# Kernel tuning notes

Hardware: AMD Instinct MI355X
Metric: run time of the kernel (lower is better)

The kernel has to match this reference:

```python
import jax, jax.numpy as jnp
import numpy as np

SINKHORN_ITERS = 20
SINKHORN_TEMP = 0.2


def log_sinkhorn(log_alpha, n_iters=SINKHORN_ITERS, temperature=SINKHORN_TEMP):
    """Log-domain Sinkhorn normalization over the last two dims."""
    log_alpha = log_alpha / temperature
    for _ in range(n_iters):
        log_alpha = log_alpha - jax.nn.logsumexp(log_alpha, axis=-1, keepdims=True)
        log_alpha = log_alpha - jax.nn.logsumexp(log_alpha, axis=-2, keepdims=True)
    return jnp.exp(log_alpha)


def setup_inputs() -> dict:
    key = jax.random.key(0)
    k_x, k_a, k_w1, k_wv = jax.random.split(key, 4)
    B = 64
    N, K, BASIS = 1024, 64, 8
    # xavier-uniform-like init scales
    a_bound = np.sqrt(6.0 / (N + N))
    w1_bound = np.sqrt(6.0 / (N + BASIS))
    wv_bound = np.sqrt(6.0 / (K + K))
    x = jax.random.normal(k_x, (B, N * K), dtype=jnp.float32)
    A_logits = jax.random.uniform(k_a, (N, N), dtype=jnp.float32, minval=-a_bound, maxval=a_bound)
    W_1 = jax.random.uniform(k_w1, (N, BASIS), dtype=jnp.float32, minval=-w1_bound, maxval=w1_bound)
    W_V = jax.random.uniform(k_wv, (BASIS, K, K), dtype=jnp.float32, minval=-wv_bound, maxval=wv_bound)
    return {"x": x, "A_logits": A_logits, "W_1": W_1, "W_V": W_V}


def reference(x, A_logits, W_1, W_V):
    B = x.shape[0]
    N, K = A_logits.shape[0], W_V.shape[-1]
    # Doubly-stochastic global mixing matrix A: [N, N]
    A = log_sinkhorn(A_logits)
    # Local block logits via basis combination: [N, K, K]
    W_logits = jnp.einsum('tk,kde->tde', W_1, W_V)
    W = log_sinkhorn(W_logits)
    x_reshaped = x.reshape(B, N, K)
    x_local = jnp.einsum('bni,nio->bno', x_reshaped, W)   # per-block KxK mix
    x_global = jnp.einsum('mn,bno->bmo', A, x_local)       # NxN block mix
    return x_global.reshape(B, N * K)
```

## Files before the change

kernel.cpp:

```cpp
#include <hip/hip_runtime.h>
#include <hip/hip_bf16.h>


#define N_DIM 1024
#define INV_T 5.0f
#define ABLK 32

typedef __attribute__((ext_vector_type(8))) short short8;
typedef __attribute__((ext_vector_type(4))) float float4v;

__device__ __forceinline__ float wave_red_sum(float x) {
#define DPP_ADD(C)                                                            \
  {                                                                           \
    int _y = __builtin_amdgcn_update_dpp(0, __float_as_int(x), (C), 0xf, 0xf, \
                                         true);                               \
    x += __int_as_float(_y);                                                  \
  }
  DPP_ADD(0x111);
  DPP_ADD(0x112);
  DPP_ADD(0x114);
  DPP_ADD(0x118);
  DPP_ADD(0x142);
  DPP_ADD(0x143);
#undef DPP_ADD
  return x;
}

__global__ __launch_bounds__(256, 2) void k_front(
    const float* __restrict__ x, const float* __restrict__ L,
    const float* __restrict__ W1, const float* __restrict__ WV,
    float* __restrict__ E0, __hip_bfloat16* __restrict__ Eh,
    __hip_bfloat16* __restrict__ El, float* __restrict__ P,
    unsigned* __restrict__ ctrl, float* __restrict__ u_g,
    float* __restrict__ v_g, float* __restrict__ XL, int write_bf16) {
  __shared__ __align__(16) float smem[5136];
  const int t = threadIdx.x;
  const int bid = blockIdx.x;
  const int lane = t & 63;
  const int w = t >> 6;
  (void)ctrl;

  if (bid < ABLK) {
    float* v_s = smem;
    float* red = smem + 1024;
    const int b = bid;
    const int r0 = b * 32;

    float e[8][16];
#pragma unroll
    for (int j = 0; j < 8; ++j) {
      const int r = r0 + 8 * w + j;
      const float* Lr = L + (size_t)r * N_DIM + lane;
#pragma unroll
      for (int k = 0; k < 16; ++k) e[j][k] = __expf(Lr[k * 64] * INV_T);
      if (write_bf16) {
        __hip_bfloat16* EhR = Eh + (size_t)r * N_DIM + lane;
        __hip_bfloat16* ElR = El + (size_t)r * N_DIM + lane;
#pragma unroll
        for (int k = 0; k < 16; ++k) {
          __hip_bfloat16 h = __float2bfloat16(e[j][k]);
          EhR[k * 64] = h;
          ElR[k * 64] = __float2bfloat16(e[j][k] - __bfloat162float(h));
        }
      } else {
        float* ER = E0 + (size_t)r * N_DIM + lane;
#pragma unroll
        for (int k = 0; k < 16; ++k) ER[k * 64] = e[j][k];
      }
    }
    v_s[t] = 1.0f;
    v_s[t + 256] = 1.0f;
    v_s[t + 512] = 1.0f;
    v_s[t + 768] = 1.0f;
    __syncthreads();

    for (int it = 0; it < 20; ++it) {
      float vv[16];
#pragma unroll
      for (int k = 0; k < 16; ++k) vv[k] = v_s[k * 64 + lane];
      float u[8];
#pragma unroll
      for (int j = 0; j < 8; ++j) {
        float p = 0.f;
#pragma unroll
        for (int k = 0; k < 16; ++k) p += e[j][k] * vv[k];
        p = wave_red_sum(p);
        u[j] = 1.0f /
               __int_as_float(__builtin_amdgcn_readlane(__float_as_int(p), 63));
      }
#pragma unroll
      for (int k = 0; k < 16; ++k) {
        float cpl = e[0][k] * u[0] + e[1][k] * u[1] + e[2][k] * u[2] +
                    e[3][k] * u[3] + e[4][k] * u[4] + e[5][k] * u[5] +
                    e[6][k] * u[6] + e[7][k] * u[7];
        red[w * 1028 + k * 64 + lane] = cpl;
      }
      if (it == 19 && lane == 0) {
#pragma unroll
        for (int j = 0; j < 8; ++j) u_g[r0 + 8 * w + j] = u[j];
      }
      __syncthreads();
      float* Pit = P + (size_t)it * (ABLK * N_DIM);
      float cp4[4];
#pragma unroll
      for (int cc = 0; cc < 4; ++cc) {
        const int c = t + cc * 256;
        cp4[cc] = red[c] + red[1028 + c] + red[2 * 1028 + c] + red[3 * 1028 + c];
        __hip_atomic_store(&Pit[b * N_DIM + c], cp4[cc], __ATOMIC_RELAXED,
                           __HIP_MEMORY_SCOPE_AGENT);
      }
      for (int cc = 0; cc < 4; ++cc) {
        const int c = t + cc * 256;
        unsigned vals[ABLK];
#pragma unroll
        for (int pb = 0; pb < ABLK; ++pb)
          vals[pb] =
              __hip_atomic_load((const unsigned*)&Pit[pb * N_DIM + c],
                                __ATOMIC_RELAXED, __HIP_MEMORY_SCOPE_AGENT);
        for (;;) {
          unsigned miss = 0u;
#pragma unroll
          for (int pb = 0; pb < ABLK; ++pb) miss |= (vals[pb] == 0u) ? 1u : 0u;
          if (miss == 0u) break;
#pragma unroll
          for (int pb = 0; pb < ABLK; ++pb)
            if (vals[pb] == 0u)
              vals[pb] = __hip_atomic_load(
                  (const unsigned*)&Pit[pb * N_DIM + c], __ATOMIC_RELAXED,
                  __HIP_MEMORY_SCOPE_AGENT);
        }
        float s2 = 0.f;
#pragma unroll
        for (int pb = 0; pb < ABLK; ++pb) s2 += __uint_as_float(vals[pb]);
        v_s[c] = 1.0f / s2;
      }
      __syncthreads();
    }
    if (b == 0) {
#pragma unroll
      for (int cc = 0; cc < 4; ++cc) v_g[t + cc * 256] = v_s[t + cc * 256];
    }
    return;
  }

  float* ug = smem + w * 64;
  const int n = (bid - ABLK) * 4 + w;

  const int pidx = lane << 2;

  float w1[8];
#pragma unroll
  for (int k = 0; k < 8; ++k) w1[k] = W1[n * 8 + k];
  float e[64];
#pragma unroll
  for (int i = 0; i < 64; ++i) {
    float acc = 0.f;
#pragma unroll
    for (int k = 0; k < 8; ++k) acc += w1[k] * WV[k * 4096 + i * 64 + lane];
    e[i] = __expf(acc * INV_T);
  }

  float v = 1.0f;
  for (int it = 0; it < 20; ++it) {
    float a[32];
    {
      const bool hi = (lane & 32) != 0;
      const int pj = pidx ^ (32 << 2);
#pragma unroll
      for (int j = 0; j < 32; ++j) {
        float s0 = (hi ? e[j] : e[j + 32]) * v;
        float k0 = (hi ? e[j + 32] : e[j]) * v;
        a[j] = k0 + __int_as_float(__builtin_amdgcn_ds_bpermute(
                        pj, __float_as_int(s0)));
      }
    }
#define BSTAGE(D)                                                          \
  {                                                                        \
    const bool hi = (lane & (D)) != 0;                                     \
    const int pj = pidx ^ ((D) << 2);                                      \
    _Pragma("unroll") for (int j = 0; j < (D); ++j) {                      \
      float s0 = hi ? a[j] : a[j + (D)];                                   \
      float k0 = hi ? a[j + (D)] : a[j];                                   \
      a[j] = k0 + __int_as_float(                                          \
                      __builtin_amdgcn_ds_bpermute(pj, __float_as_int(s0))); \
    }                                                                      \
  }
    BSTAGE(16)
    BSTAGE(8)
    BSTAGE(4)
    BSTAGE(2)
    BSTAGE(1)
#undef BSTAGE
    const float u_l = 1.0f / a[0];
    ug[lane] = u_l;
    float s2 = 0.f;
#pragma unroll
    for (int q = 0; q < 16; ++q) {
      float4 u4 = *(const float4*)&ug[4 * q];
      s2 += e[4 * q] * u4.x + e[4 * q + 1] * u4.y + e[4 * q + 2] * u4.z +
            e[4 * q + 3] * u4.w;
    }
    v = 1.0f / s2;
  }

#pragma unroll
  for (int q = 0; q < 16; ++q) {
    float4 u4 = *(const float4*)&ug[4 * q];
    e[4 * q] *= u4.x;
    e[4 * q + 1] *= u4.y;
    e[4 * q + 2] *= u4.z;
    e[4 * q + 3] *= u4.w;
  }

  const float* xn = x + (size_t)n * 64;
  float* xl = XL + (size_t)n * 4096;
#pragma unroll 4
  for (int bb = 0; bb < 64; ++bb) {
    const float* xr = xn + (size_t)bb * 65536;
    float acc = 0.f;
#pragma unroll
    for (int q = 0; q < 16; ++q) {
      float4 xb = *(const float4*)&xr[4 * q];
      acc += xb.x * e[4 * q] + xb.y * e[4 * q + 1] + xb.z * e[4 * q + 2] +
             xb.w * e[4 * q + 3];
    }
    xl[bb * 64 + lane] = acc * v;
  }
}

__global__ __launch_bounds__(256) void k_xt(const float* __restrict__ XL,
                                            const float* __restrict__ v_g,
                                            __hip_bfloat16* __restrict__ XTh,
                                            __hip_bfloat16* __restrict__ XTl) {
  __shared__ float T[64 * 68];
  __shared__ float vsh[64];
  const int t = threadIdx.x;
  const int n0 = blockIdx.x * 64;
  const int c0 = blockIdx.y * 64;
  if (t < 64) vsh[t] = v_g[n0 + t];
  {
    const int r = t >> 4;
    const int c4 = (t & 15) * 4;
#pragma unroll
    for (int p = 0; p < 4; ++p) {
      float4 f =
          *(const float4*)&XL[(size_t)(n0 + r + 16 * p) * 4096 + c0 + c4];
      *(float4*)&T[(r + 16 * p) * 68 + c4] = f;
    }
  }
  __syncthreads();
  const int cl = t >> 2;
  const int nb = (t & 3) * 16;
  __align__(16) __hip_bfloat16 hbuf[16];
  __align__(16) __hip_bfloat16 lbuf[16];
#pragma unroll
  for (int j = 0; j < 16; ++j) {
    float xv = T[(nb + j) * 68 + cl] * vsh[nb + j];
    __hip_bfloat16 h = __float2bfloat16(xv);
    hbuf[j] = h;
    lbuf[j] = __float2bfloat16(xv - __bfloat162float(h));
  }
  const size_t off = (size_t)(c0 + cl) * 1024 + n0 + nb;
  *(uint4*)&XTh[off] = *(uint4*)&hbuf[0];
  *(uint4*)&XTh[off + 8] = *(uint4*)&hbuf[8];
  *(uint4*)&XTl[off] = *(uint4*)&lbuf[0];
  *(uint4*)&XTl[off + 8] = *(uint4*)&lbuf[8];
}

#define LSTR 72
__global__ __launch_bounds__(256) void k_gemm3(
    const ushort* __restrict__ Eh, const ushort* __restrict__ El,
    const ushort* __restrict__ XTh, const ushort* __restrict__ XTl,
    const float* __restrict__ u_g, float* __restrict__ out) {
  __shared__ ushort As[128 * LSTR];
  __shared__ ushort Xs[128 * LSTR];
  __shared__ float ush[128];
  const int t = threadIdx.x;
  const int m0 = blockIdx.x * 128;
  const int c0 = blockIdx.y * 128;
  const int wid = t >> 6, lane = t & 63;
  const int wm = (wid & 1) * 64, wc = (wid >> 1) * 64;
  const int lm = lane & 15, q = lane >> 4;
  const int sr = t >> 1;
  const int sc = (t & 1) * 32;
  if (t < 128) ush[t] = u_g[m0 + t];

  float4v acc[4][4];
#pragma unroll
  for (int i = 0; i < 4; ++i)
#pragma unroll
    for (int j = 0; j < 4; ++j) acc[i][j] = (float4v){0.f, 0.f, 0.f, 0.f};

  for (int seg = 0; seg < 3; ++seg) {
    const ushort* Ag = (seg == 1) ? El : Eh;
    const ushort* Xg = (seg == 2) ? XTl : XTh;
    for (int k0 = 0; k0 < 1024; k0 += 64) {
      __syncthreads();
      const ushort* ag = Ag + (size_t)(m0 + sr) * 1024 + k0 + sc;
      const ushort* xg = Xg + (size_t)(c0 + sr) * 1024 + k0 + sc;
      uint4 a0 = *(const uint4*)(ag);
      uint4 a1 = *(const uint4*)(ag + 8);
      uint4 a2 = *(const uint4*)(ag + 16);
      uint4 a3 = *(const uint4*)(ag + 24);
      uint4 x0 = *(const uint4*)(xg);
      uint4 x1 = *(const uint4*)(xg + 8);
      uint4 x2 = *(const uint4*)(xg + 16);
      uint4 x3 = *(const uint4*)(xg + 24);
      *(uint4*)&As[sr * LSTR + sc] = a0;
      *(uint4*)&As[sr * LSTR + sc + 8] = a1;
      *(uint4*)&As[sr * LSTR + sc + 16] = a2;
      *(uint4*)&As[sr * LSTR + sc + 24] = a3;
      *(uint4*)&Xs[sr * LSTR + sc] = x0;
      *(uint4*)&Xs[sr * LSTR + sc + 8] = x1;
      *(uint4*)&Xs[sr * LSTR + sc + 16] = x2;
      *(uint4*)&Xs[sr * LSTR + sc + 24] = x3;
      __syncthreads();
#pragma unroll
      for (int kk = 0; kk < 2; ++kk) {
        short8 af[4], xf[4];
#pragma unroll
        for (int i = 0; i < 4; ++i)
          af[i] = *(const short8*)&As[(wm + 16 * i + lm) * LSTR + kk * 32 +
                                      q * 8];
#pragma unroll
        for (int j = 0; j < 4; ++j)
          xf[j] = *(const short8*)&Xs[(wc + 16 * j + lm) * LSTR + kk * 32 +
                                      q * 8];
#pragma unroll
        for (int i = 0; i < 4; ++i)
#pragma unroll
          for (int j = 0; j < 4; ++j)
            acc[i][j] = __builtin_amdgcn_mfma_f32_16x16x32_bf16(
                af[i], xf[j], acc[i][j], 0, 0, 0);
      }
    }
  }
#pragma unroll
  for (int i = 0; i < 4; ++i) {
#pragma unroll
    for (int j = 0; j < 4; ++j) {
      const int ml = wm + 16 * i + q * 4;
      const int m = m0 + ml;
      const int c = c0 + wc + 16 * j + lm;
      const int bb = c >> 6, o = c & 63;
      float* dst = out + (size_t)bb * 65536 + (size_t)m * 64 + o;
#pragma unroll
      for (int r = 0; r < 4; ++r) dst[64 * r] = acc[i][j][r] * ush[ml + r];
    }
  }
}

__global__ __launch_bounds__(256) void k_gemm(const float* __restrict__ E0,
                                              const float* __restrict__ XL,
                                              const float* __restrict__ u_g,
                                              const float* __restrict__ v_g,
                                              float* __restrict__ out) {
  __shared__ float Asm[32][132];
  __shared__ float Xsm[32][132];
  const int t = threadIdx.x;
  const int m0 = blockIdx.x * 128;
  const int c0 = blockIdx.y * 128;
  const int my8 = (t >> 4) * 8;
  const int cx8 = (t & 15) * 8;
  const int kk = t & 31;
  const int rr = t >> 5;
  float acc[8][8] = {};

  for (int k0 = 0; k0 < 1024; k0 += 32) {
#pragma unroll
    for (int s = 0; s < 16; ++s)
      Asm[kk][rr + 8 * s] = E0[(size_t)(m0 + rr + 8 * s) * 1024 + k0 + kk];
#pragma unroll
    for (int s = 0; s < 4; ++s) {
      const int krow = k0 + rr + 8 * s;
      float vk = v_g[krow];
      float4 f = *(const float4*)&XL[(size_t)krow * 4096 + c0 + kk * 4];
      f.x *= vk;
      f.y *= vk;
      f.z *= vk;
      f.w *= vk;
      *(float4*)&Xsm[rr + 8 * s][kk * 4] = f;
    }
    __syncthreads();
#pragma unroll
    for (int k = 0; k < 32; ++k) {
      float a[8], xv[8];
      *(float4*)&a[0] = *(const float4*)&Asm[k][my8];
      *(float4*)&a[4] = *(const float4*)&Asm[k][my8 + 4];
      *(float4*)&xv[0] = *(const float4*)&Xsm[k][cx8];
      *(float4*)&xv[4] = *(const float4*)&Xsm[k][cx8 + 4];
#pragma unroll
      for (int i = 0; i < 8; ++i)
#pragma unroll
        for (int j = 0; j < 8; ++j) acc[i][j] += a[i] * xv[j];
    }
    __syncthreads();
  }

#pragma unroll
  for (int i = 0; i < 8; ++i) {
    const int m = m0 + my8 + i;
    const float um = u_g[m];
    const int c = c0 + cx8;
    const int bb = c >> 6, o = c & 63;
    float* dst = out + (size_t)bb * 65536 + (size_t)m * 64 + o;
#pragma unroll
    for (int j = 0; j < 8; ++j) dst[j] = acc[i][j] * um;
  }
}

extern "C" void kernel_launch(void* const* d_in, const int* in_sizes, int n_in,
                              void* d_out, int out_size, void* d_ws,
                              size_t ws_size, hipStream_t stream) {
  (void)in_sizes;
  (void)n_in;
  (void)out_size;
  const float* x = (const float*)d_in[0];
  const float* Alog = (const float*)d_in[1];
  const float* W1 = (const float*)d_in[2];
  const float* WV = (const float*)d_in[3];
  float* out = (float*)d_out;

  char* ws = (char*)d_ws;
  const size_t MB = 1024 * 1024;
  const size_t KB = 1024;
  const bool use_bf16 = ws_size >= (40 * MB + 256 * KB);
  const size_t P_BYTES = 20ull * ABLK * N_DIM * sizeof(float);

  float* E0;
  float* XL;
  float* P;
  float* u_g;
  float* v_g;
  unsigned* ctrl;
  __hip_bfloat16 *Eh = nullptr, *El = nullptr, *XTh = nullptr, *XTl = nullptr;
  if (use_bf16) {
    P = (float*)(ws);
    E0 = (float*)(ws);
    XL = (float*)(ws + 4 * MB);
    Eh = (__hip_bfloat16*)(ws + 20 * MB);
    El = (__hip_bfloat16*)(ws + 22 * MB);
    XTh = (__hip_bfloat16*)(ws + 24 * MB);
    XTl = (__hip_bfloat16*)(ws + 32 * MB);
    u_g = (float*)(ws + 40 * MB);
    v_g = (float*)(ws + 40 * MB + 4 * KB);
    ctrl = (unsigned*)(ws + 40 * MB + 8 * KB);
  } else {
    E0 = (float*)(ws);
    XL = (float*)(ws + 4 * MB);
    P = (float*)(ws + 20 * MB);
    u_g = (float*)(ws + 20 * MB + 2560 * KB);
    v_g = (float*)(ws + 20 * MB + 2564 * KB);
    ctrl = (unsigned*)(ws + 20 * MB + 2568 * KB);
  }

  hipMemsetAsync(P, 0, P_BYTES, stream);
  hipLaunchKernelGGL(k_front, dim3(ABLK + 256), dim3(256), 0, stream, x, Alog,
                     W1, WV, E0, Eh, El, P, ctrl, u_g, v_g, XL,
                     use_bf16 ? 1 : 0);
  if (use_bf16) {
    hipLaunchKernelGGL(k_xt, dim3(16, 64), dim3(256), 0, stream, XL, v_g, XTh,
                       XTl);
    hipLaunchKernelGGL(k_gemm3, dim3(8, 32), dim3(256), 0, stream,
                       (const ushort*)Eh, (const ushort*)El, (const ushort*)XTh,
                       (const ushort*)XTl, u_g, out);
  } else {
    hipLaunchKernelGGL(k_gemm, dim3(8, 32), dim3(256), 0, stream, E0, XL, u_g,
                       v_g, out);
  }
}
```

Measured before the change: 299.8 us.

## Fold Sinkhorn scalings into bf16 A and double-buffer GEMM via direct LDS loads

The A-matrix Sinkhorn blocks now write the fully scaled doubly-stochastic matrix (e*u*v) as bf16 hi/lo pairs after the iterations, instead of raw exp values. This removes the v scaling from the transpose kernel and the u scaling from the GEMM epilogue. The GEMM is restructured into a single 48-step loop with double-buffered LDS tiles filled by global_load_lds, overlapping loads with MFMA. The padded LDS stride is dropped, which may introduce bank conflicts, and the bf16 writes move to the end of the Sinkhorn blocks, lengthening their tail.

```diff
diff --git a/kernel.cpp b/kernel.cpp
--- a/kernel.cpp
+++ b/kernel.cpp
@@ -26,11 +26,17 @@
   return x;
 }
 
+__device__ __forceinline__ void stage16(const ushort* g, ushort* l) {
+  __builtin_amdgcn_global_load_lds(
+      (const __attribute__((address_space(1))) void*)g,
+      (__attribute__((address_space(3))) void*)l, 16, 0, 0);
+}
+
 __global__ __launch_bounds__(256, 2) void k_front(
     const float* __restrict__ x, const float* __restrict__ L,
     const float* __restrict__ W1, const float* __restrict__ WV,
-    float* __restrict__ E0, __hip_bfloat16* __restrict__ Eh,
-    __hip_bfloat16* __restrict__ El, float* __restrict__ P,
+    float* __restrict__ E0, __hip_bfloat16* __restrict__ Mh,
+    __hip_bfloat16* __restrict__ Ml, float* __restrict__ P,
     unsigned* __restrict__ ctrl, float* __restrict__ u_g,
     float* __restrict__ v_g, float* __restrict__ XL, int write_bf16) {
   __shared__ __align__(16) float smem[5136];
@@ -53,16 +59,7 @@
       const float* Lr = L + (size_t)r * N_DIM + lane;
 #pragma unroll
       for (int k = 0; k < 16; ++k) e[j][k] = __expf(Lr[k * 64] * INV_T);
-      if (write_bf16) {
-        __hip_bfloat16* EhR = Eh + (size_t)r * N_DIM + lane;
-        __hip_bfloat16* ElR = El + (size_t)r * N_DIM + lane;
-#pragma unroll
-        for (int k = 0; k < 16; ++k) {
-          __hip_bfloat16 h = __float2bfloat16(e[j][k]);
-          EhR[k * 64] = h;
-          ElR[k * 64] = __float2bfloat16(e[j][k] - __bfloat162float(h));
-        }
-      } else {
+      if (!write_bf16) {
         float* ER = E0 + (size_t)r * N_DIM + lane;
 #pragma unroll
         for (int k = 0; k < 16; ++k) ER[k * 64] = e[j][k];
@@ -74,6 +71,7 @@
     v_s[t + 768] = 1.0f;
     __syncthreads();
 
+    float uF[8];
     for (int it = 0; it < 20; ++it) {
       float vv[16];
 #pragma unroll
@@ -87,6 +85,10 @@
         p = wave_red_sum(p);
         u[j] = 1.0f /
                __int_as_float(__builtin_amdgcn_readlane(__float_as_int(p), 63));
+      }
+      if (it == 19) {
+#pragma unroll
+        for (int j = 0; j < 8; ++j) uF[j] = u[j];
       }
 #pragma unroll
       for (int k = 0; k < 16; ++k) {
@@ -95,18 +97,14 @@
                     e[6][k] * u[6] + e[7][k] * u[7];
         red[w * 1028 + k * 64 + lane] = cpl;
       }
-      if (it == 19 && lane == 0) {
-#pragma unroll
-        for (int j = 0; j < 8; ++j) u_g[r0 + 8 * w + j] = u[j];
-      }
       __syncthreads();
       float* Pit = P + (size_t)it * (ABLK * N_DIM);
-      float cp4[4];
 #pragma unroll
       for (int cc = 0; cc < 4; ++cc) {
         const int c = t + cc * 256;
-        cp4[cc] = red[c] + red[1028 + c] + red[2 * 1028 + c] + red[3 * 1028 + c];
-        __hip_atomic_store(&Pit[b * N_DIM + c], cp4[cc], __ATOMIC_RELAXED,
+        float cp =
+            red[c] + red[1028 + c] + red[2 * 1028 + c] + red[3 * 1028 + c];
+        __hip_atomic_store(&Pit[b * N_DIM + c], cp, __ATOMIC_RELAXED,
                            __HIP_MEMORY_SCOPE_AGENT);
       }
       for (int cc = 0; cc < 4; ++cc) {
@@ -136,9 +134,28 @@
       }
       __syncthreads();
     }
+    if (lane == 0) {
+#pragma unroll
+      for (int j = 0; j < 8; ++j) u_g[r0 + 8 * w + j] = uF[j];
+    }
     if (b == 0) {
 #pragma unroll
       for (int cc = 0; cc < 4; ++cc) v_g[t + cc * 256] = v_s[t + cc * 256];
+    }
+    if (write_bf16) {
+#pragma unroll
+      for (int j = 0; j < 8; ++j) {
+        const int r = r0 + 8 * w + j;
+        __hip_bfloat16* MhR = Mh + (size_t)r * N_DIM + lane;
+        __hip_bfloat16* MlR = Ml + (size_t)r * N_DIM + lane;
+#pragma unroll
+        for (int k = 0; k < 16; ++k) {
+          float m = e[j][k] * uF[j] * v_s[k * 64 + lane];
+          __hip_bfloat16 h = __float2bfloat16(m);
+          MhR[k * 64] = h;
+          MlR[k * 64] = __float2bfloat16(m - __bfloat162float(h));
+        }
+      }
     }
     return;
   }
@@ -229,15 +246,12 @@
 }
 
 __global__ __launch_bounds__(256) void k_xt(const float* __restrict__ XL,
-                                            const float* __restrict__ v_g,
                                             __hip_bfloat16* __restrict__ XTh,
                                             __hip_bfloat16* __restrict__ XTl) {
   __shared__ float T[64 * 68];
-  __shared__ float vsh[64];
   const int t = threadIdx.x;
   const int n0 = blockIdx.x * 64;
   const int c0 = blockIdx.y * 64;
-  if (t < 64) vsh[t] = v_g[n0 + t];
   {
     const int r = t >> 4;
     const int c4 = (t & 15) * 4;
@@ -255,7 +269,7 @@
   __align__(16) __hip_bfloat16 lbuf[16];
 #pragma unroll
   for (int j = 0; j < 16; ++j) {
-    float xv = T[(nb + j) * 68 + cl] * vsh[nb + j];
+    float xv = T[(nb + j) * 68 + cl];
     __hip_bfloat16 h = __float2bfloat16(xv);
     hbuf[j] = h;
     lbuf[j] = __float2bfloat16(xv - __bfloat162float(h));
@@ -267,23 +281,21 @@
   *(uint4*)&XTl[off + 8] = *(uint4*)&lbuf[8];
 }
 
-#define LSTR 72
-__global__ __launch_bounds__(256) void k_gemm3(
-    const ushort* __restrict__ Eh, const ushort* __restrict__ El,
+__global__ __launch_bounds__(256, 2) void k_gemm3(
+    const ushort* __restrict__ Mh, const ushort* __restrict__ Ml,
     const ushort* __restrict__ XTh, const ushort* __restrict__ XTl,
-    const float* __restrict__ u_g, float* __restrict__ out) {
-  __shared__ ushort As[128 * LSTR];
-  __shared__ ushort Xs[128 * LSTR];
-  __shared__ float ush[128];
+    float* __restrict__ out) {
+  __shared__ __align__(16) ushort As[2][128 * 64];
+  __shared__ __align__(16) ushort Xs[2][128 * 64];
   const int t = threadIdx.x;
   const int m0 = blockIdx.x * 128;
   const int c0 = blockIdx.y * 128;
   const int wid = t >> 6, lane = t & 63;
   const int wm = (wid & 1) * 64, wc = (wid >> 1) * 64;
   const int lm = lane & 15, q = lane >> 4;
-  const int sr = t >> 1;
-  const int sc = (t & 1) * 32;
-  if (t < 128) ush[t] = u_g[m0 + t];
+  const int g_row = wid * 8 + (lane >> 3);
+  const int g_col = (lane & 7) * 8;
+  const int l_off = wid * 512;
 
   float4v acc[4][4];
 #pragma unroll
@@ -291,61 +303,57 @@
 #pragma unroll
     for (int j = 0; j < 4; ++j) acc[i][j] = (float4v){0.f, 0.f, 0.f, 0.f};
 
-  for (int seg = 0; seg < 3; ++seg) {
-    const ushort* Ag = (seg == 1) ? El : Eh;
-    const ushort* Xg = (seg == 2) ? XTl : XTh;
-    for (int k0 = 0; k0 < 1024; k0 += 64) {
-      __syncthreads();
-      const ushort* ag = Ag + (size_t)(m0 + sr) * 1024 + k0 + sc;
-      const ushort* xg = Xg + (size_t)(c0 + sr) * 1024 + k0 + sc;
-      uint4 a0 = *(const uint4*)(ag);
-      uint4 a1 = *(const uint4*)(ag + 8);
-      uint4 a2 = *(const uint4*)(ag + 16);
-      uint4 a3 = *(const uint4*)(ag + 24);
-      uint4 x0 = *(const uint4*)(xg);
-      uint4 x1 = *(const uint4*)(xg + 8);
-      uint4 x2 = *(const uint4*)(xg + 16);
-      uint4 x3 = *(const uint4*)(xg + 24);
-      *(uint4*)&As[sr * LSTR + sc] = a0;
-      *(uint4*)&As[sr * LSTR + sc + 8] = a1;
-      *(uint4*)&As[sr * LSTR + sc + 16] = a2;
-      *(uint4*)&As[sr * LSTR + sc + 24] = a3;
-      *(uint4*)&Xs[sr * LSTR + sc] = x0;
-      *(uint4*)&Xs[sr * LSTR + sc + 8] = x1;
-      *(uint4*)&Xs[sr * LSTR + sc + 16] = x2;
-      *(uint4*)&Xs[sr * LSTR + sc + 24] = x3;
-      __syncthreads();
-#pragma unroll
-      for (int kk = 0; kk < 2; ++kk) {
-        short8 af[4], xf[4];
-#pragma unroll
-        for (int i = 0; i < 4; ++i)
-          af[i] = *(const short8*)&As[(wm + 16 * i + lm) * LSTR + kk * 32 +
-                                      q * 8];
+#define STAGE(BUF, SS)                                                       \
+  {                                                                          \
+    const int seg_ = (SS) >> 4;                                              \
+    const int k0_ = ((SS) & 15) * 64;                                        \
+    const ushort* Ag_ = (seg_ == 1) ? Ml : Mh;                               \
+    const ushort* Xg_ = (seg_ == 2) ? XTl : XTh;                             \
+    _Pragma("unroll") for (int r = 0; r < 4; ++r) {                          \
+      stage16(Ag_ + (size_t)(m0 + r * 32 + g_row) * 1024 + k0_ + g_col,      \
+              &As[BUF][r * 2048 + l_off]);                                   \
+      stage16(Xg_ + (size_t)(c0 + r * 32 + g_row) * 1024 + k0_ + g_col,      \
+              &Xs[BUF][r * 2048 + l_off]);                                   \
+    }                                                                        \
+  }
+
+  STAGE(0, 0);
+  __syncthreads();
+  for (int s = 0; s < 48; ++s) {
+    const int cur = s & 1;
+    if (s + 1 < 48) STAGE(cur ^ 1, s + 1);
+#pragma unroll
+    for (int kk = 0; kk < 2; ++kk) {
+      short8 af[4], xf[4];
+#pragma unroll
+      for (int i = 0; i < 4; ++i)
+        af[i] =
+            *(const short8*)&As[cur][(wm + 16 * i + lm) * 64 + kk * 32 + q * 8];
+#pragma unroll
+      for (int j = 0; j < 4; ++j)
+        xf[j] =
+            *(const short8*)&Xs[cur][(wc + 16 * j + lm) * 64 + kk * 32 + q * 8];
+#pragma unroll
+      for (int i = 0; i < 4; ++i)
 #pragma unroll
         for (int j = 0; j < 4; ++j)
-          xf[j] = *(const short8*)&Xs[(wc + 16 * j + lm) * LSTR + kk * 32 +
-                                      q * 8];
-#pragma unroll
-        for (int i = 0; i < 4; ++i)
-#pragma unroll
-          for (int j = 0; j < 4; ++j)
-            acc[i][j] = __builtin_amdgcn_mfma_f32_16x16x32_bf16(
-                af[i], xf[j], acc[i][j], 0, 0, 0);
-      }
-    }
-  }
+          acc[i][j] = __builtin_amdgcn_mfma_f32_16x16x32_bf16(
+              af[i], xf[j], acc[i][j], 0, 0, 0);
+    }
+    __syncthreads();
+  }
+#undef STAGE
+
 #pragma unroll
   for (int i = 0; i < 4; ++i) {
 #pragma unroll
     for (int j = 0; j < 4; ++j) {
-      const int ml = wm + 16 * i + q * 4;
-      const int m = m0 + ml;
+      const int m = m0 + wm + 16 * i + q * 4;
       const int c = c0 + wc + 16 * j + lm;
       const int bb = c >> 6, o = c & 63;
       float* dst = out + (size_t)bb * 65536 + (size_t)m * 64 + o;
 #pragma unroll
-      for (int r = 0; r < 4; ++r) dst[64 * r] = acc[i][j][r] * ush[ml + r];
+      for (int r = 0; r < 4; ++r) dst[64 * r] = acc[i][j][r];
     }
   }
 }
@@ -433,13 +441,13 @@
   float* u_g;
   float* v_g;
   unsigned* ctrl;
-  __hip_bfloat16 *Eh = nullptr, *El = nullptr, *XTh = nullptr, *XTl = nullptr;
+  __hip_bfloat16 *Mh = nullptr, *Ml = nullptr, *XTh = nullptr, *XTl = nullptr;
   if (use_bf16) {
     P = (float*)(ws);
     E0 = (float*)(ws);
     XL = (float*)(ws + 4 * MB);
-    Eh = (__hip_bfloat16*)(ws + 20 * MB);
-    El = (__hip_bfloat16*)(ws + 22 * MB);
+    Mh = (__hip_bfloat16*)(ws + 20 * MB);
+    Ml = (__hip_bfloat16*)(ws + 22 * MB);
     XTh = (__hip_bfloat16*)(ws + 24 * MB);
     XTl = (__hip_bfloat16*)(ws + 32 * MB);
     u_g = (float*)(ws + 40 * MB);
@@ -456,14 +464,13 @@
 
   hipMemsetAsync(P, 0, P_BYTES, stream);
   hipLaunchKernelGGL(k_front, dim3(ABLK + 256), dim3(256), 0, stream, x, Alog,
-                     W1, WV, E0, Eh, El, P, ctrl, u_g, v_g, XL,
+                     W1, WV, E0, Mh, Ml, P, ctrl, u_g, v_g, XL,
                      use_bf16 ? 1 : 0);
   if (use_bf16) {
-    hipLaunchKernelGGL(k_xt, dim3(16, 64), dim3(256), 0, stream, XL, v_g, XTh,
-                       XTl);
+    hipLaunchKernelGGL(k_xt, dim3(16, 64), dim3(256), 0, stream, XL, XTh, XTl);
     hipLaunchKernelGGL(k_gemm3, dim3(8, 32), dim3(256), 0, stream,
-                       (const ushort*)Eh, (const ushort*)El, (const ushort*)XTh,
-                       (const ushort*)XTl, u_g, out);
+                       (const ushort*)Mh, (const ushort*)Ml, (const ushort*)XTh,
+                       (const ushort*)XTl, out);
   } else {
     hipLaunchKernelGGL(k_gemm, dim3(8, 32), dim3(256), 0, stream, E0, XL, u_g,
                        v_g, out);
```

Result: slower. 317.5 us (+5.9%).
